# Kernel optimization log

Hardware: AMD Instinct MI355X
Metric: run time of the kernel (lower is better)

The kernel has to match this reference:

```python
import jax, jax.numpy as jnp
import numpy as np

B, T, N, F, G, H, E, S = 8, 50, 1000, 4, 32, 256, 32000, 5
IN0 = G * N  # LSTM layer-0 input size


def setup_inputs() -> dict:
    key = jax.random.key(0)
    ks = jax.random.split(key, 16)
    sc = 0.02
    return {
        "x_sequences": jax.random.normal(ks[0], (B, T, N, F), jnp.float32),
        "edge_indices": jax.random.randint(ks[1], (B, T, 2, E), 0, N),
        "edge_weights": jax.random.uniform(ks[2], (B, T, E), jnp.float32),
        "W_gcn": jax.random.normal(ks[3], (F, G), jnp.float32) * sc,
        "b_gcn": jnp.zeros((G,), jnp.float32),
        "Wih0": jax.random.normal(ks[4], (4 * H, IN0), jnp.float32) * sc,
        "Whh0": jax.random.normal(ks[5], (4 * H, H), jnp.float32) * sc,
        "bih0": jnp.zeros((4 * H,), jnp.float32),
        "bhh0": jnp.zeros((4 * H,), jnp.float32),
        "Wih1": jax.random.normal(ks[6], (4 * H, H), jnp.float32) * sc,
        "Whh1": jax.random.normal(ks[7], (4 * H, H), jnp.float32) * sc,
        "bih1": jnp.zeros((4 * H,), jnp.float32),
        "bhh1": jnp.zeros((4 * H,), jnp.float32),
        "fc_W": jax.random.normal(ks[8], (S * N * F, H), jnp.float32) * sc,
        "fc_b": jnp.zeros((S * N * F,), jnp.float32),
    }


def _lstm_layer(seq, Wih, Whh, bih, bhh):
    # seq: [B, T, in]; PyTorch gate order i, f, g, o
    b, h = seq.shape[0], Whh.shape[1]

    def step(carry, x_t):
        hs, cs = carry
        gates = x_t @ Wih.T + bih + hs @ Whh.T + bhh
        i, f, g, o = jnp.split(gates, 4, axis=-1)
        c = jax.nn.sigmoid(f) * cs + jax.nn.sigmoid(i) * jnp.tanh(g)
        hn = jax.nn.sigmoid(o) * jnp.tanh(c)
        return (hn, c), hn

    init = (jnp.zeros((b, h), seq.dtype), jnp.zeros((b, h), seq.dtype))
    _, hs = jax.lax.scan(step, init, jnp.swapaxes(seq, 0, 1))
    return jnp.swapaxes(hs, 0, 1)  # [B, T, H]


def reference(x_sequences, edge_indices, edge_weights, W_gcn, b_gcn,
              Wih0, Whh0, bih0, bhh0, Wih1, Whh1, bih1, bhh1, fc_W, fc_b):
    # --- spatial: weighted GCN per (batch, timestep) graph ---
    def gcn_one(x, ei, ew):
        xw = x @ W_gcn                       # [N, G]
        msg = ew[:, None] * xw[ei[0]]        # gather src, scale by edge weight
        agg = jnp.zeros_like(xw).at[ei[1]].add(msg)  # scatter-add to dst
        return agg + b_gcn

    z = jax.vmap(jax.vmap(gcn_one))(x_sequences, edge_indices, edge_weights)  # [B,T,N,G]
    z = jnp.tanh(z.reshape(B, T, N * G))

    # --- temporal: 2-layer LSTM (dropout off / eval mode), last hidden ---
    h1 = _lstm_layer(z, Wih0, Whh0, bih0, bhh0)
    h2 = _lstm_layer(h1, Wih1, Whh1, bih1, bhh1)
    last = h2[:, -1]  # [B, H]

    # --- prediction head ---
    pred = jnp.tanh(last) @ fc_W.T + fc_b
    return pred.reshape(B, S, N, F)  # squeeze(-1) is a no-op since F > 1
```

## Files before the change

### kernel.cpp

```cpp
#include <hip/hip_runtime.h>
#include <math.h>

#define B_ 8
#define T_ 50
#define N_ 1000
#define F_ 4
#define G_ 32
#define H_ 256
#define E_ 32000
#define S_ 5
#define R_ 400
#define K0_ 32000
#define NG_ 1024
#define KS_ 16

#define L0_WGS 8
#define L1_WGS 16

typedef unsigned int uint_;
typedef unsigned short ushort_;
typedef unsigned long long u64_;
typedef __attribute__((ext_vector_type(8))) short bf16x8;
typedef __attribute__((ext_vector_type(4))) float f32x4;

static __device__ __forceinline__ float sigm(float x) { return 1.0f / (1.0f + expf(-x)); }

static __device__ __forceinline__ ushort_ f2bf(float x) {
  uint_ u = __float_as_uint(x);
  u += 0x7FFFu + ((u >> 16) & 1u);
  return (ushort_)(u >> 16);
}
static __device__ __forceinline__ float bf2f(ushort_ b) {
  return __uint_as_float(((uint_)b) << 16);
}
static __device__ __forceinline__ uint_ pk2(float a, float b) {
  return (uint_)f2bf(a) | ((uint_)f2bf(b) << 16);
}
static __device__ __forceinline__ float resid(float x) {
  return x - bf2f(f2bf(x));
}
static __device__ __forceinline__ void split8(const float* v, bf16x8* hi, bf16x8* lo) {
  bf16x8 h8, l8;
#pragma unroll
  for (int j = 0; j < 8; ++j) {
    ushort_ hb = f2bf(v[j]);
    h8[j] = (short)hb;
    l8[j] = (short)f2bf(v[j] - bf2f(hb));
  }
  *hi = h8; *lo = l8;
}

static __device__ __forceinline__ void gload_lds16(const void* g, void* l) {
  __builtin_amdgcn_global_load_lds(
      (const __attribute__((address_space(1))) uint_*)g,
      (__attribute__((address_space(3))) uint_*)l, 16, 0, 0);
}

__global__ __launch_bounds__(512, 8) void gcn_scatter(
    const float* __restrict__ x, const int* __restrict__ ei,
    const float* __restrict__ ew, float* __restrict__ P) {
  __shared__ float xs[N_ * 4];
  __shared__ float aggX[N_ * 4];
  const int r = blockIdx.x >> 1;
  const int eh = blockIdx.x & 1;
  const int tid = threadIdx.x;

  const float4* xg = (const float4*)(x + (size_t)r * N_ * F_);
  float4* xs4 = (float4*)xs;
  for (int i = tid; i < N_; i += 512) xs4[i] = xg[i];
  float4* av = (float4*)aggX;
  for (int i = tid; i < N_; i += 512) av[i] = make_float4(0.f, 0.f, 0.f, 0.f);
  __syncthreads();

  const int* src = ei + (size_t)r * 2 * E_;
  const int* dst = src + E_;
  const float* wp = ew + (size_t)r * E_;

  const int f = tid & 3;
  const int es = tid >> 2;
  const int e0 = eh * (E_ / 2);
  const int e1 = e0 + (E_ / 2);
  for (int e = e0 + es; e < e1; e += 128) {
    const int s = src[e], d = dst[e];
    const float m = wp[e] * xs[(s << 2) | f];
    unsafeAtomicAdd(&aggX[(d << 2) | f], m);
  }
  __syncthreads();

  float4* pv = (float4*)(P + (size_t)blockIdx.x * (N_ * 4));
  for (int i = tid; i < N_; i += 512) pv[i] = av[i];
}

__global__ __launch_bounds__(256) void gcn_transform(
    const float* __restrict__ P, const float* __restrict__ Wg,
    const float* __restrict__ bg, ushort_* __restrict__ Zh,
    ushort_* __restrict__ Zl) {
  __shared__ float mm[N_ * 4];
  __shared__ float wg[128];
  __shared__ float bgl[32];
  const int r = blockIdx.x;
  const int tid = threadIdx.x;
  const float* P0 = P + (size_t)(2 * r) * (N_ * 4);
  const float* P1 = P0 + N_ * 4;
  for (int i = tid; i < N_ * 4; i += 256) mm[i] = P0[i] + P1[i];
  if (tid < 128) wg[tid] = Wg[tid];
  if (tid < 32) bgl[tid] = bg[tid];
  __syncthreads();

  const int s = (r >> 1) & 3;
  ushort_* zhr = Zh + (size_t)r * K0_;
  ushort_* zlr = Zl + (size_t)r * K0_;
  for (int q = tid; q < 4000; q += 256) {
    const int n = q >> 2, gb = q & 3;
    const float4 a = *(const float4*)&mm[n << 2];
    float z[8];
#pragma unroll
    for (int j = 0; j < 8; ++j) {
      const int g = gb * 8 + j;
      z[j] = tanhf(bgl[g] + a.x * wg[g] + a.y * wg[32 + g] + a.z * wg[64 + g] +
                   a.w * wg[96 + g]);
    }
    uint4 vh, vl;
    vh.x = pk2(z[0], z[1]); vh.y = pk2(z[2], z[3]);
    vh.z = pk2(z[4], z[5]); vh.w = pk2(z[6], z[7]);
    vl.x = pk2(resid(z[0]), resid(z[1])); vl.y = pk2(resid(z[2]), resid(z[3]));
    vl.z = pk2(resid(z[4]), resid(z[5])); vl.w = pk2(resid(z[6]), resid(z[7]));
    const size_t off = (size_t)n * 32 + ((size_t)(gb ^ s) << 3);
    *(uint4*)&zhr[off] = vh;
    *(uint4*)&zlr[off] = vl;
  }
}

__global__ __launch_bounds__(256, 2) void gemm_x3(
    const ushort_* __restrict__ Zh, const ushort_* __restrict__ Zl,
    const float* __restrict__ W, float* __restrict__ part) {
  const int mt = blockIdx.x;
  const int nt = blockIdx.y;
  const int kz = blockIdx.z;
  const int k0 = (kz < 8) ? kz * 2016 : 16128 + (kz - 8) * 1984;
  const int nsteps = (kz < 8) ? 63 : 62;

  __shared__ __align__(16) ushort_ Ah[128 * 32];
  __shared__ __align__(16) ushort_ Al[128 * 32];
  __shared__ __align__(16) ushort_ Bh[128 * 32];
  __shared__ __align__(16) ushort_ Bl[128 * 32];

  const int tid = threadIdx.x;
  const int lane = tid & 63, wv = tid >> 6;
  const int wr = wv >> 1, wc = wv & 1;

  const int ar0 = tid >> 2, ap = tid & 3;
  const int ar1 = 64 + (tid >> 2);
  const ushort_* zh0 = Zh + (size_t)(mt * 128 + ar0) * K0_ + k0 + ap * 8;
  const ushort_* zh1 = Zh + (size_t)(mt * 128 + ar1) * K0_ + k0 + ap * 8;
  const ushort_* zl0 = Zl + (size_t)(mt * 128 + ar0) * K0_ + k0 + ap * 8;
  const ushort_* zl1 = Zl + (size_t)(mt * 128 + ar1) * K0_ + k0 + ap * 8;

  const int bn = tid >> 1, bh2 = tid & 1;
  const int sB = (bn >> 1) & 3;
  const int q0 = (bh2 * 2) ^ sB, q1 = (bh2 * 2 + 1) ^ sB;
  const float* wrow = W + (size_t)(nt * 128 + bn) * K0_ + k0 + bh2 * 16;

  f32x4 acc[4][4];
#pragma unroll
  for (int i = 0; i < 4; ++i)
#pragma unroll
    for (int j = 0; j < 4; ++j) acc[i][j] = (f32x4){0.f, 0.f, 0.f, 0.f};

  for (int st = 0; st < nsteps; ++st) {
    gload_lds16(zh0, &Ah[(size_t)tid * 8]);
    gload_lds16(zh1, &Ah[2048 + (size_t)tid * 8]);
    gload_lds16(zl0, &Al[(size_t)tid * 8]);
    gload_lds16(zl1, &Al[2048 + (size_t)tid * 8]);
    zh0 += 32; zh1 += 32; zl0 += 32; zl1 += 32;

    const float4 w0 = *(const float4*)(wrow);
    const float4 w1 = *(const float4*)(wrow + 4);
    const float4 w2 = *(const float4*)(wrow + 8);
    const float4 w3 = *(const float4*)(wrow + 12);
    wrow += 32;
    uint4 ha, hb, la, lb;
    ha.x = pk2(w0.x, w0.y); ha.y = pk2(w0.z, w0.w);
    ha.z = pk2(w1.x, w1.y); ha.w = pk2(w1.z, w1.w);
    la.x = pk2(resid(w0.x), resid(w0.y)); la.y = pk2(resid(w0.z), resid(w0.w));
    la.z = pk2(resid(w1.x), resid(w1.y)); la.w = pk2(resid(w1.z), resid(w1.w));
    hb.x = pk2(w2.x, w2.y); hb.y = pk2(w2.z, w2.w);
    hb.z = pk2(w3.x, w3.y); hb.w = pk2(w3.z, w3.w);
    lb.x = pk2(resid(w2.x), resid(w2.y)); lb.y = pk2(resid(w2.z), resid(w2.w));
    lb.z = pk2(resid(w3.x), resid(w3.y)); lb.w = pk2(resid(w3.z), resid(w3.w));
    *(uint4*)&Bh[bn * 32 + q0 * 8] = ha;
    *(uint4*)&Bh[bn * 32 + q1 * 8] = hb;
    *(uint4*)&Bl[bn * 32 + q0 * 8] = la;
    *(uint4*)&Bl[bn * 32 + q1 * 8] = lb;

    __syncthreads();

    bf16x8 afh[4], afl[4], bfh[4], bfl[4];
#pragma unroll
    for (int i = 0; i < 4; ++i) {
      const int arow = wr * 64 + i * 16 + (lane & 15);
      const int aq = (lane >> 4) ^ ((arow >> 1) & 3);
      afh[i] = *(const bf16x8*)&Ah[arow * 32 + aq * 8];
      afl[i] = *(const bf16x8*)&Al[arow * 32 + aq * 8];
      const int brow = wc * 64 + i * 16 + (lane & 15);
      const int bq = (lane >> 4) ^ ((brow >> 1) & 3);
      bfh[i] = *(const bf16x8*)&Bh[brow * 32 + bq * 8];
      bfl[i] = *(const bf16x8*)&Bl[brow * 32 + bq * 8];
    }
#pragma unroll
    for (int i = 0; i < 4; ++i)
#pragma unroll
      for (int j = 0; j < 4; ++j) {
        acc[i][j] = __builtin_amdgcn_mfma_f32_16x16x32_bf16(afh[i], bfh[j], acc[i][j], 0, 0, 0);
        acc[i][j] = __builtin_amdgcn_mfma_f32_16x16x32_bf16(afh[i], bfl[j], acc[i][j], 0, 0, 0);
        acc[i][j] = __builtin_amdgcn_mfma_f32_16x16x32_bf16(afl[i], bfh[j], acc[i][j], 0, 0, 0);
      }
    __syncthreads();
  }

  const int crow0 = mt * 128 + wr * 64 + ((lane >> 4) << 2);
  const int ccol = nt * 128 + wc * 64 + (lane & 15);
  float* pbase = part + (size_t)kz * R_ * NG_;
#pragma unroll
  for (int i = 0; i < 4; ++i)
#pragma unroll
    for (int rr = 0; rr < 4; ++rr) {
      const int gr = crow0 + i * 16 + rr;
      if (gr < R_) {
#pragma unroll
        for (int j = 0; j < 4; ++j)
          pbase[(size_t)gr * NG_ + ccol + j * 16] = acc[i][j][rr];
      }
    }
}

__global__ __launch_bounds__(256) void reduce_kernel(
    const float* __restrict__ part, const float* __restrict__ bih0,
    const float* __restrict__ bhh0, float* __restrict__ G0) {
  const int idx = blockIdx.x * 256 + threadIdx.x;
  if (idx >= R_ * NG_) return;
  const int n = idx & (NG_ - 1);
  float s = bih0[n] + bhh0[n];
#pragma unroll
  for (int ks = 0; ks < KS_; ++ks) s += part[(size_t)ks * R_ * NG_ + idx];
  G0[idx] = s;
}

__device__ __forceinline__ void wait_cnt_rlx(unsigned* p, unsigned want) {
  unsigned tries = 0;
  while (__hip_atomic_load(p, __ATOMIC_RELAXED, __HIP_MEMORY_SCOPE_AGENT) < want) {
    __builtin_amdgcn_s_sleep(1);
    if (++tries > (1u << 24)) break;
  }
}

__global__ __launch_bounds__(256, 1) void recur2(
    const float* __restrict__ G0, const float* __restrict__ Whh0,
    const float* __restrict__ Wih1, const float* __restrict__ Whh1,
    const float* __restrict__ bih1, const float* __restrict__ bhh1,
    uint_* __restrict__ h1p, uint_* __restrict__ h2p, float* __restrict__ h2f,
    unsigned* __restrict__ cnt0, unsigned* __restrict__ cnt1) {
  const int wg = blockIdx.x;
  const int tid = threadIdx.x;
  const bool is1 = wg >= L0_WGS;
  const int w = is1 ? wg - L0_WGS : wg;
  const int lane = tid & 63;
  const int wv = tid >> 6;

  __shared__ __align__(16) ushort_ AfH[16 * 64 * 8];
  __shared__ __align__(16) ushort_ AfL[16 * 64 * 8];
  __shared__ float gates[4 * 8 * 32];
  __shared__ float cs[256];

  bf16x8 BH[16], BL[16];
  if (!is1) {
#pragma unroll
    for (int nt2 = 0; nt2 < 2; ++nt2) {
      const int n = wv * 256 + w * 32 + nt2 * 16 + (lane & 15);
      const float* wr = Whh0 + (size_t)n * 256 + (lane >> 4) * 8;
#pragma unroll
      for (int s = 0; s < 8; ++s) {
        float v[8];
        *(float4*)&v[0] = *(const float4*)(wr + s * 32);
        *(float4*)&v[4] = *(const float4*)(wr + s * 32 + 4);
        split8(v, &BH[nt2 * 8 + s], &BL[nt2 * 8 + s]);
      }
    }
  } else {
    const int n = wv * 256 + w * 16 + (lane & 15);
    const float* wr1 = Wih1 + (size_t)n * 256 + (lane >> 4) * 8;
    const float* wr2 = Whh1 + (size_t)n * 256 + (lane >> 4) * 8;
#pragma unroll
    for (int s = 0; s < 16; ++s) {
      const float* wr = (s < 8) ? (wr1 + s * 32) : (wr2 + (s - 8) * 32);
      float v[8];
      *(float4*)&v[0] = *(const float4*)wr;
      *(float4*)&v[4] = *(const float4*)(wr + 4);
      split8(v, &BH[s], &BL[s]);
    }
  }

  {
    uint_* a32 = (uint_*)AfH;
    uint_* b32 = (uint_*)AfL;
    for (int i = tid; i < 4096; i += 256) { a32[i] = 0u; b32[i] = 0u; }
    cs[tid] = 0.f;
  }
  float bias1 = 0.f;
  if (is1) {
    const int n = wv * 256 + w * 16 + (lane & 15);
    bias1 = bih1[n] + bhh1[n];
  }
  __syncthreads();

  for (int t = 0; t < T_; ++t) {
    float g0v[2][4];
    if (!is1) {
#pragma unroll
      for (int nt2 = 0; nt2 < 2; ++nt2)
#pragma unroll
        for (int rr = 0; rr < 4; ++rr) {
          const int m = (lane >> 4) * 4 + rr;
          g0v[nt2][rr] = (m < 8)
              ? G0[(size_t)(m * T_ + t) * NG_ + wv * 256 + w * 32 + nt2 * 16 + (lane & 15)]
              : 0.f;
        }
    }
    if (tid == 0) {
      if (!is1) {
        if (t > 0) wait_cnt_rlx(&cnt0[t - 1], L0_WGS);
      } else {
        wait_cnt_rlx(&cnt0[t], L0_WGS);
        if (t > 0) wait_cnt_rlx(&cnt1[t - 1], L1_WGS);
      }
    }
    __syncthreads();

    if (!is1) {
      const int m = tid >> 5, c8 = tid & 31;
      const u64_* src = (const u64_*)(h1p + (size_t)t * 2048 + m * 256 + c8 * 8);
      u64_ d[4];
#pragma unroll
      for (int p = 0; p < 4; ++p)
        d[p] = __hip_atomic_load(src + p, __ATOMIC_RELAXED, __HIP_MEMORY_SCOPE_AGENT);
      bf16x8 hh, hl;
#pragma unroll
      for (int p = 0; p < 4; ++p) {
        const uint_ v0 = (uint_)d[p], v1 = (uint_)(d[p] >> 32);
        hh[p * 2] = (short)(v0 & 0xffffu); hl[p * 2] = (short)(v0 >> 16);
        hh[p * 2 + 1] = (short)(v1 & 0xffffu); hl[p * 2 + 1] = (short)(v1 >> 16);
      }
      const int s = c8 >> 2, sub = c8 & 3, ln = m + sub * 16;
      *(bf16x8*)&AfH[(s * 64 + ln) * 8] = hh;
      *(bf16x8*)&AfL[(s * 64 + ln) * 8] = hl;
    } else {
#pragma unroll
      for (int cc = 0; cc < 2; ++cc) {
        const int c = tid + cc * 256;
        const int m = c >> 6, c8 = c & 63, k = c8 * 8;
        const uint_* bp = (k < 256) ? (h1p + (size_t)(t + 1) * 2048 + m * 256 + k)
                                    : (h2p + (size_t)t * 2048 + m * 256 + (k - 256));
        const u64_* src = (const u64_*)bp;
        u64_ d[4];
#pragma unroll
        for (int p = 0; p < 4; ++p)
          d[p] = __hip_atomic_load(src + p, __ATOMIC_RELAXED, __HIP_MEMORY_SCOPE_AGENT);
        bf16x8 hh, hl;
#pragma unroll
        for (int p = 0; p < 4; ++p) {
          const uint_ v0 = (uint_)d[p], v1 = (uint_)(d[p] >> 32);
          hh[p * 2] = (short)(v0 & 0xffffu); hl[p * 2] = (short)(v0 >> 16);
          hh[p * 2 + 1] = (short)(v1 & 0xffffu); hl[p * 2 + 1] = (short)(v1 >> 16);
        }
        const int s = c8 >> 2, sub = c8 & 3, ln = m + sub * 16;
        *(bf16x8*)&AfH[(s * 64 + ln) * 8] = hh;
        *(bf16x8*)&AfL[(s * 64 + ln) * 8] = hl;
      }
    }
    __syncthreads();

    f32x4 acc0 = (f32x4){0.f, 0.f, 0.f, 0.f};
    f32x4 acc1 = (f32x4){0.f, 0.f, 0.f, 0.f};
    if (!is1) {
#pragma unroll
      for (int s = 0; s < 8; ++s) {
        const bf16x8 ah = *(const bf16x8*)&AfH[(s * 64 + lane) * 8];
        const bf16x8 al = *(const bf16x8*)&AfL[(s * 64 + lane) * 8];
        acc0 = __builtin_amdgcn_mfma_f32_16x16x32_bf16(ah, BH[s], acc0, 0, 0, 0);
        acc0 = __builtin_amdgcn_mfma_f32_16x16x32_bf16(ah, BL[s], acc0, 0, 0, 0);
        acc0 = __builtin_amdgcn_mfma_f32_16x16x32_bf16(al, BH[s], acc0, 0, 0, 0);
        acc1 = __builtin_amdgcn_mfma_f32_16x16x32_bf16(ah, BH[8 + s], acc1, 0, 0, 0);
        acc1 = __builtin_amdgcn_mfma_f32_16x16x32_bf16(ah, BL[8 + s], acc1, 0, 0, 0);
        acc1 = __builtin_amdgcn_mfma_f32_16x16x32_bf16(al, BH[8 + s], acc1, 0, 0, 0);
      }
    } else {
#pragma unroll
      for (int s = 0; s < 16; ++s) {
        const bf16x8 ah = *(const bf16x8*)&AfH[(s * 64 + lane) * 8];
        const bf16x8 al = *(const bf16x8*)&AfL[(s * 64 + lane) * 8];
        acc0 = __builtin_amdgcn_mfma_f32_16x16x32_bf16(ah, BH[s], acc0, 0, 0, 0);
        acc0 = __builtin_amdgcn_mfma_f32_16x16x32_bf16(ah, BL[s], acc0, 0, 0, 0);
        acc0 = __builtin_amdgcn_mfma_f32_16x16x32_bf16(al, BH[s], acc0, 0, 0, 0);
      }
    }

    if (!is1) {
#pragma unroll
      for (int rr = 0; rr < 4; ++rr) {
        const int m = (lane >> 4) * 4 + rr;
        if (m < 8) {
          gates[(wv * 8 + m) * 32 + (lane & 15)] = acc0[rr] + g0v[0][rr];
          gates[(wv * 8 + m) * 32 + 16 + (lane & 15)] = acc1[rr] + g0v[1][rr];
        }
      }
    } else {
#pragma unroll
      for (int rr = 0; rr < 4; ++rr) {
        const int m = (lane >> 4) * 4 + rr;
        if (m < 8) gates[(wv * 8 + m) * 16 + (lane & 15)] = acc0[rr] + bias1;
      }
    }
    __syncthreads();

    if (!is1) {
      const int m = tid >> 5, j = tid & 31;
      const float gi = gates[(0 * 8 + m) * 32 + j];
      const float gf = gates[(1 * 8 + m) * 32 + j];
      const float gg = gates[(2 * 8 + m) * 32 + j];
      const float go = gates[(3 * 8 + m) * 32 + j];
      float c = sigm(gf) * cs[tid] + sigm(gi) * tanhf(gg);
      cs[tid] = c;
      const float h = sigm(go) * tanhf(c);
      const ushort_ hh = f2bf(h);
      const ushort_ hl = f2bf(h - bf2f(hh));
      __hip_atomic_store(h1p + (size_t)(t + 1) * 2048 + m * 256 + w * 32 + j,
                         (uint_)hh | ((uint_)hl << 16), __ATOMIC_RELAXED,
                         __HIP_MEMORY_SCOPE_AGENT);
    } else if (tid < 128) {
      const int m = tid >> 4, j = tid & 15;
      const float gi = gates[(0 * 8 + m) * 16 + j];
      const float gf = gates[(1 * 8 + m) * 16 + j];
      const float gg = gates[(2 * 8 + m) * 16 + j];
      const float go = gates[(3 * 8 + m) * 16 + j];
      float c = sigm(gf) * cs[tid] + sigm(gi) * tanhf(gg);
      cs[tid] = c;
      const float h = sigm(go) * tanhf(c);
      const ushort_ hh = f2bf(h);
      const ushort_ hl = f2bf(h - bf2f(hh));
      __hip_atomic_store(h2p + (size_t)(t + 1) * 2048 + m * 256 + w * 16 + j,
                         (uint_)hh | ((uint_)hl << 16), __ATOMIC_RELAXED,
                         __HIP_MEMORY_SCOPE_AGENT);
      if (t == T_ - 1) h2f[m * 256 + w * 16 + j] = h;
    }
    __syncthreads();
    if (tid == 0) {
      __hip_atomic_fetch_add(is1 ? &cnt1[t] : &cnt0[t], 1u, __ATOMIC_RELEASE,
                             __HIP_MEMORY_SCOPE_AGENT);
    }
  }
}

__global__ __launch_bounds__(256) void fc_kernel(
    const float* __restrict__ h2last, const float* __restrict__ fcW,
    const float* __restrict__ fcb, float* __restrict__ out) {
  __shared__ float tl[2048];
  const int tid = threadIdx.x;
  for (int i = tid; i < 2048; i += 256) tl[i] = tanhf(h2last[i]);
  __syncthreads();
  const int nidx = blockIdx.x * 256 + tid;
  if (nidx >= S_ * N_ * F_) return;
  float accv[8];
#pragma unroll
  for (int m2 = 0; m2 < 8; ++m2) accv[m2] = 0.f;
  const float* wr = fcW + (size_t)nidx * 256;
  for (int k = 0; k < 256; k += 4) {
    float4 w4 = *(const float4*)(wr + k);
#pragma unroll
    for (int m2 = 0; m2 < 8; ++m2) {
      float4 t4 = *(const float4*)&tl[m2 * 256 + k];
      accv[m2] += w4.x * t4.x + w4.y * t4.y + w4.z * t4.z + w4.w * t4.w;
    }
  }
  const float bv = fcb[nidx];
#pragma unroll
  for (int m2 = 0; m2 < 8; ++m2) out[(size_t)m2 * (S_ * N_ * F_) + nidx] = accv[m2] + bv;
}

extern "C" void kernel_launch(void* const* d_in, const int* in_sizes, int n_in,
                              void* d_out, int out_size, void* d_ws, size_t ws_size,
                              hipStream_t stream) {
  const float* x    = (const float*)d_in[0];
  const int*   ei   = (const int*)d_in[1];
  const float* ew   = (const float*)d_in[2];
  const float* Wg   = (const float*)d_in[3];
  const float* bg   = (const float*)d_in[4];
  const float* Wih0 = (const float*)d_in[5];
  const float* Whh0 = (const float*)d_in[6];
  const float* bih0 = (const float*)d_in[7];
  const float* bhh0 = (const float*)d_in[8];
  const float* Wih1 = (const float*)d_in[9];
  const float* Whh1 = (const float*)d_in[10];
  const float* bih1 = (const float*)d_in[11];
  const float* bhh1 = (const float*)d_in[12];
  const float* fcW  = (const float*)d_in[13];
  const float* fcb  = (const float*)d_in[14];
  float* out = (float*)d_out;
  float* ws = (float*)d_ws;

  ushort_* Zh = (ushort_*)ws;
  ushort_* Zl = (ushort_*)(ws + 6400000);
  float* part = ws + 12800000;
  float* G0   = ws + 19353600;
  uint_* h1p  = (uint_*)(ws + 19763200);
  uint_* h2p  = (uint_*)(ws + 19867648);
  unsigned* cnt0 = (unsigned*)(ws + 19972096);
  unsigned* cnt1 = cnt0 + 64;
  float* h2f  = part;

  hipMemsetAsync(h1p, 0, (size_t)(104448 * 2 + 128) * sizeof(float), stream);

  gcn_scatter<<<R_ * 2, 512, 0, stream>>>(x, ei, ew, part);
  gcn_transform<<<R_, 256, 0, stream>>>(part, Wg, bg, Zh, Zl);
  gemm_x3<<<dim3(4, 8, KS_), 256, 0, stream>>>(Zh, Zl, Wih0, part);
  reduce_kernel<<<(R_ * NG_ + 255) / 256, 256, 0, stream>>>(part, bih0, bhh0, G0);
  recur2<<<L0_WGS + L1_WGS, 256, 0, stream>>>(G0, Whh0, Wih1, Whh1, bih1, bhh1,
                                              h1p, h2p, h2f, cnt0, cnt1);
  fc_kernel<<<(S_ * N_ * F_ + 255) / 256, 256, 0, stream>>>(h2f, fcW, fcb, out);
}
```

Before: 908.0 us.

## Double-buffer edge lists into LDS and vectorize GCN scatter with swizzled atomics

```diff
diff --git a/kernel.cpp b/kernel.cpp
--- a/kernel.cpp
+++ b/kernel.cpp
@@ -17,6 +17,10 @@
 #define L0_WGS 8
 #define L1_WGS 16
 
+#define ECHUNK 2048
+#define EHALF (E_ / 2)
+#define NCHUNK ((EHALF + ECHUNK - 1) / ECHUNK)
+
 typedef unsigned int uint_;
 typedef unsigned short ushort_;
 typedef unsigned long long u64_;
@@ -56,39 +60,78 @@
       (__attribute__((address_space(3))) uint_*)l, 16, 0, 0);
 }
 
-__global__ __launch_bounds__(512, 8) void gcn_scatter(
+__global__ __launch_bounds__(512, 4) void gcn_scatter(
     const float* __restrict__ x, const int* __restrict__ ei,
     const float* __restrict__ ew, float* __restrict__ P) {
-  __shared__ float xs[N_ * 4];
-  __shared__ float aggX[N_ * 4];
+  __shared__ __align__(16) float xs[N_ * 4];
+  __shared__ __align__(16) float aggX[N_ * 4];
+  __shared__ __align__(16) int   sb[2][ECHUNK];
+  __shared__ __align__(16) int   db[2][ECHUNK];
+  __shared__ __align__(16) float wb[2][ECHUNK];
   const int r = blockIdx.x >> 1;
   const int eh = blockIdx.x & 1;
   const int tid = threadIdx.x;
 
-  const float4* xg = (const float4*)(x + (size_t)r * N_ * F_);
-  float4* xs4 = (float4*)xs;
-  for (int i = tid; i < N_; i += 512) xs4[i] = xg[i];
-  float4* av = (float4*)aggX;
-  for (int i = tid; i < N_; i += 512) av[i] = make_float4(0.f, 0.f, 0.f, 0.f);
+  const int* srcp = ei + (size_t)r * 2 * E_ + eh * EHALF;
+  const int* dstp = ei + (size_t)r * 2 * E_ + E_ + eh * EHALF;
+  const float* ewp = ew + (size_t)r * E_ + eh * EHALF;
+
+  const float* xrow = x + (size_t)r * (N_ * F_);
+  if (tid < 500) {
+    gload_lds16(xrow + tid * 4, &xs[tid * 4]);
+    gload_lds16(xrow + (500 + tid) * 4, &xs[(500 + tid) * 4]);
+  }
+  {
+    float4* av = (float4*)aggX;
+    for (int i = tid; i < N_; i += 512) av[i] = make_float4(0.f, 0.f, 0.f, 0.f);
+  }
+  {
+    const int cnt = (EHALF < ECHUNK) ? EHALF : ECHUNK;
+    if (tid < (cnt >> 2)) {
+      gload_lds16(srcp + tid * 4, &sb[0][tid * 4]);
+      gload_lds16(dstp + tid * 4, &db[0][tid * 4]);
+      gload_lds16(ewp + tid * 4, &wb[0][tid * 4]);
+    }
+  }
   __syncthreads();
 
-  const int* src = ei + (size_t)r * 2 * E_;
-  const int* dst = src + E_;
-  const float* wp = ew + (size_t)r * E_;
-
-  const int f = tid & 3;
-  const int es = tid >> 2;
-  const int e0 = eh * (E_ / 2);
-  const int e1 = e0 + (E_ / 2);
-  for (int e = e0 + es; e < e1; e += 128) {
-    const int s = src[e], d = dst[e];
-    const float m = wp[e] * xs[(s << 2) | f];
-    unsafeAtomicAdd(&aggX[(d << 2) | f], m);
-  }
-  __syncthreads();
+  int cur = 0;
+  for (int c = 0; c < NCHUNK; ++c) {
+    if (c + 1 < NCHUNK) {
+      const int base = (c + 1) * ECHUNK;
+      const int cnt = EHALF - base < ECHUNK ? EHALF - base : ECHUNK;
+      const int nxt = cur ^ 1;
+      if (tid < (cnt >> 2)) {
+        gload_lds16(srcp + base + tid * 4, &sb[nxt][tid * 4]);
+        gload_lds16(dstp + base + tid * 4, &db[nxt][tid * 4]);
+        gload_lds16(ewp + base + tid * 4, &wb[nxt][tid * 4]);
+      }
+    }
+    const int cnt = EHALF - c * ECHUNK < ECHUNK ? EHALF - c * ECHUNK : ECHUNK;
+    for (int i = tid; i < cnt; i += 512) {
+      const int s = sb[cur][i], d = db[cur][i];
+      const float w = wb[cur][i];
+      const float4 xv = *(const float4*)&xs[s << 2];
+      const int swz = (d >> 3) & 3;
+      unsafeAtomicAdd(&aggX[(d << 2) | swz], w * xv.x);
+      unsafeAtomicAdd(&aggX[(d << 2) | (1 ^ swz)], w * xv.y);
+      unsafeAtomicAdd(&aggX[(d << 2) | (2 ^ swz)], w * xv.z);
+      unsafeAtomicAdd(&aggX[(d << 2) | (3 ^ swz)], w * xv.w);
+    }
+    __syncthreads();
+    cur ^= 1;
+  }
 
   float4* pv = (float4*)(P + (size_t)blockIdx.x * (N_ * 4));
-  for (int i = tid; i < N_; i += 512) pv[i] = av[i];
+  for (int i = tid; i < N_; i += 512) {
+    const int swz = (i >> 3) & 3;
+    float4 v;
+    v.x = aggX[(i << 2) | swz];
+    v.y = aggX[(i << 2) | (1 ^ swz)];
+    v.z = aggX[(i << 2) | (2 ^ swz)];
+    v.w = aggX[(i << 2) | (3 ^ swz)];
+    pv[i] = v;
+  }
 }
 
 __global__ __launch_bounds__(256) void gcn_transform(
```

Measured after the change: 919.1 us. About the same (+1.2%).
